# Performance work log

Measured on AMD Instinct MI355X. Metric: run time of the kernel, lower is better.

Reference implementation:

```python
import jax, jax.numpy as jnp
import numpy as np

# ---- Cl(4,1) blade algebra (CGA for 3D Euclidean space) ----
_METRIC = [1.0, 1.0, 1.0, 1.0, -1.0]  # e1..e4 square +1, e5 squares -1

def _popcount(x):
    return bin(x).count('1')

def _blade_mul(a, b):
    # sign from reordering basis vectors into canonical order
    s = 0
    t = a >> 1
    while t:
        s += _popcount(t & b)
        t >>= 1
    sign = -1.0 if (s & 1) else 1.0
    shared = a & b
    for i in range(5):
        if (shared >> i) & 1:
            sign *= _METRIC[i]
    return a ^ b, sign

_EVEN = [b for b in range(32) if _popcount(b) % 2 == 0]   # 16 even blades (versor)
_ODD = [b for b in range(32) if _popcount(b) % 2 == 1]    # 16 odd blades
_G1 = [1, 2, 4, 8, 16]                                    # grade-1 blades (CGA point)
_ODD_IDX = {b: i for i, b in enumerate(_ODD)}
_G1_IDX = {b: i for i, b in enumerate(_G1)}

def _rev_sign(b):
    g = _popcount(b)
    return -1.0 if (g * (g - 1) // 2) % 2 else 1.0

# Sparse Cayley structure tensors for the sandwich product M X ~M
_T1 = np.zeros((16, 5, 16), np.float32)   # even * grade1 -> odd
for _ie, _a in enumerate(_EVEN):
    for _ip, _b in enumerate(_G1):
        _c, _s = _blade_mul(_a, _b)
        _T1[_ie, _ip, _ODD_IDX[_c]] = _s
_T2 = np.zeros((16, 16, 5), np.float32)   # odd * reverse(even) -> grade-1
for _io, _a in enumerate(_ODD):
    for _ie, _b in enumerate(_EVEN):
        _c, _s = _blade_mul(_a, _b)
        if _c in _G1_IDX:
            _T2[_io, _ie, _G1_IDX[_c]] = _s * _rev_sign(_b)
T1 = jnp.asarray(_T1)
T2 = jnp.asarray(_T2)

N_POINTS = 2097152  # 2^21 points

def setup_inputs() -> dict:
    key = jax.random.key(0)
    k1, k2 = jax.random.split(key)
    x = jax.random.normal(k1, (N_POINTS, 3), dtype=jnp.float32)
    versor = 0.1 * jax.random.normal(k2, (N_POINTS, 16), dtype=jnp.float32)
    versor = versor.at[:, 0].add(1.0)  # near-identity even versor (scalar blade is index 0)
    return {"versor": versor, "x": x}

def _cga_encode(x):
    # P = x + 0.5|x|^2 e_inf + e_0, with e_inf = e4+e5, e_0 = (e5-e4)/2
    half_sq = 0.5 * jnp.sum(x * x, axis=-1, keepdims=True)
    return jnp.concatenate([x, half_sq - 0.5, half_sq + 0.5], axis=-1)  # (..., 5)

def _sandwich(versor, point):
    mx = jnp.einsum('...e,...p,epo->...o', versor, point, T1)   # M X : odd, 16 comps
    return jnp.einsum('...o,...e,oeq->...q', mx, versor, T2)    # (M X) ~M : grade-1, 5 comps

def _cga_decode(p):
    # scale = -P . e_inf = p[e5] - p[e4]; euclidean = P_xyz / scale
    s = p[..., 4:5] - p[..., 3:4]
    return p[..., :3] / s

def reference(versor, x):
    original_dtype = x.dtype
    xf = x.astype(jnp.float32)
    vf = versor.astype(jnp.float32)
    point = _cga_encode(xf)
    transformed = _sandwich(vf, point)
    return _cga_decode(transformed).astype(original_dtype)
```

## Files before the change

kernel.cpp:

```cpp
#include <hip/hip_runtime.h>
#include <utility>


namespace cga {

__host__ __device__ constexpr int popc5(int x) {
    int c = 0;
    for (int i = 0; i < 5; ++i) c += (x >> i) & 1;
    return c;
}
__host__ __device__ constexpr int blade_of_even(int idx) {
    int cnt = 0;
    for (int b = 0; b < 32; ++b)
        if ((popc5(b) & 1) == 0) { if (cnt == idx) return b; ++cnt; }
    return 0;
}
__host__ __device__ constexpr int blade_of_odd(int idx) {
    int cnt = 0;
    for (int b = 0; b < 32; ++b)
        if ((popc5(b) & 1) == 1) { if (cnt == idx) return b; ++cnt; }
    return 0;
}
__host__ __device__ constexpr int even_index(int blade) {
    int idx = 0;
    for (int b = 0; b < blade; ++b) if ((popc5(b) & 1) == 0) ++idx;
    return idx;
}
__host__ __device__ constexpr int odd_index(int blade) {
    int idx = 0;
    for (int b = 0; b < blade; ++b) if ((popc5(b) & 1) == 1) ++idx;
    return idx;
}
__host__ __device__ constexpr int mul_sign(int a, int b) {
    int s = 0;
    for (int t = a >> 1; t; t >>= 1) s += popc5(t & b);
    int sign = (s & 1) ? -1 : 1;
    if ((a & b) & 16) sign = -sign;
    return sign;
}
__host__ __device__ constexpr int rev_sign(int b) {
    int g = popc5(b);
    return ((g * (g - 1) / 2) & 1) ? -1 : 1;
}

struct Tables {
    int t1_dst[16][5];
    int t1_sgn[16][5];
    int t2_e[16][5];
    int t2_sgn[16][5];
};

__host__ __device__ constexpr Tables make_tables() {
    Tables r{};
    for (int ie = 0; ie < 16; ++ie) {
        const int a = blade_of_even(ie);
        for (int ip = 0; ip < 5; ++ip) {
            const int b = 1 << ip;
            const int c = a ^ b;
            r.t1_dst[ie][ip] = odd_index(c);
            r.t1_sgn[ie][ip] = mul_sign(a, b);
        }
    }
    for (int io = 0; io < 16; ++io) {
        const int a = blade_of_odd(io);
        for (int iq = 0; iq < 5; ++iq) {
            const int c = 1 << iq;
            const int b = a ^ c;
            r.t2_e[io][iq]   = even_index(b);
            r.t2_sgn[io][iq] = mul_sign(a, b) * rev_sign(b);
        }
    }
    return r;
}

constexpr Tables TAB = make_tables();

}

template <int IE, int IP>
__device__ __forceinline__ void t1_term(const float (&v)[16], const float (&p)[5],
                                        float (&mx)[16]) {
    constexpr int dst = cga::TAB.t1_dst[IE][IP];
    constexpr int sgn = cga::TAB.t1_sgn[IE][IP];
    if constexpr (sgn >= 0) mx[dst] = __builtin_fmaf( v[IE], p[IP], mx[dst]);
    else                    mx[dst] = __builtin_fmaf(-v[IE], p[IP], mx[dst]);
}
template <std::size_t... I>
__device__ __forceinline__ void t1_all(const float (&v)[16], const float (&p)[5],
                                       float (&mx)[16], std::index_sequence<I...>) {
    (t1_term<(int)(I / 5), (int)(I % 5)>(v, p, mx), ...);
}
template <int IO, int IQ>
__device__ __forceinline__ void t2_term(const float (&v)[16], const float (&mx)[16],
                                        float (&q)[5]) {
    constexpr int e   = cga::TAB.t2_e[IO][IQ];
    constexpr int sgn = cga::TAB.t2_sgn[IO][IQ];
    if constexpr (sgn >= 0) q[IQ] = __builtin_fmaf( mx[IO], v[e], q[IQ]);
    else                    q[IQ] = __builtin_fmaf(-mx[IO], v[e], q[IQ]);
}
template <std::size_t... I>
__device__ __forceinline__ void t2_all(const float (&v)[16], const float (&mx)[16],
                                       float (&q)[5], std::index_sequence<I...>) {
    (t2_term<(int)(I / 5), (int)(I % 5)>(v, mx, q), ...);
}

__device__ __forceinline__ void cga_compute(const float (&v)[16],
                                            float x0, float x1, float x2,
                                            float& o0, float& o1, float& o2) {
    const float hs = 0.5f * (x0 * x0 + x1 * x1 + x2 * x2);
    const float p[5] = {x0, x1, x2, hs - 0.5f, hs + 0.5f};
    float mx[16] = {};
    t1_all(v, p, mx, std::make_index_sequence<16 * 5>{});
    float q[5] = {};
    t2_all(v, mx, q, std::make_index_sequence<16 * 5>{});
    const float inv = 1.0f / (q[4] - q[3]);
    o0 = q[0] * inv;
    o1 = q[1] * inv;
    o2 = q[2] * inv;
}

template <int PPT>
__global__ __launch_bounds__(256) void cga_aos_kernel(
    const float* __restrict__ versor,
    const float* __restrict__ x,
    float* __restrict__ out,
    int stride_pts)
{
    const int tid = blockIdx.x * blockDim.x + threadIdx.x;

    float4 f[PPT][4];
    float  xv[PPT][3];
#pragma unroll
    for (int k = 0; k < PPT; ++k) {
        const size_t p = (size_t)tid + (size_t)k * stride_pts;
        const float4* vp = reinterpret_cast<const float4*>(versor) + p * 4;
        f[k][0] = vp[0];
        f[k][1] = vp[1];
        f[k][2] = vp[2];
        f[k][3] = vp[3];
        xv[k][0] = x[3 * p + 0];
        xv[k][1] = x[3 * p + 1];
        xv[k][2] = x[3 * p + 2];
    }

#pragma unroll
    for (int k = 0; k < PPT; ++k) {
        const float v[16] = {f[k][0].x, f[k][0].y, f[k][0].z, f[k][0].w,
                             f[k][1].x, f[k][1].y, f[k][1].z, f[k][1].w,
                             f[k][2].x, f[k][2].y, f[k][2].z, f[k][2].w,
                             f[k][3].x, f[k][3].y, f[k][3].z, f[k][3].w};
        float o0, o1, o2;
        cga_compute(v, xv[k][0], xv[k][1], xv[k][2], o0, o1, o2);
        const size_t p = (size_t)tid + (size_t)k * stride_pts;
        out[3 * p + 0] = o0;
        out[3 * p + 1] = o1;
        out[3 * p + 2] = o2;
    }
}

__global__ __launch_bounds__(256) void cga_simple_kernel(
    const float* __restrict__ versor,
    const float* __restrict__ x,
    float* __restrict__ out,
    int n)
{
    const int i = blockIdx.x * blockDim.x + threadIdx.x;
    if (i >= n) return;
    const float4* v4 = reinterpret_cast<const float4*>(versor) + (size_t)i * 4;
    const float4 a0 = v4[0], a1 = v4[1], a2 = v4[2], a3 = v4[3];
    const float v[16] = {a0.x, a0.y, a0.z, a0.w, a1.x, a1.y, a1.z, a1.w,
                         a2.x, a2.y, a2.z, a2.w, a3.x, a3.y, a3.z, a3.w};
    float o0, o1, o2;
    cga_compute(v, x[(size_t)3 * i], x[(size_t)3 * i + 1], x[(size_t)3 * i + 2],
                o0, o1, o2);
    out[(size_t)3 * i + 0] = o0;
    out[(size_t)3 * i + 1] = o1;
    out[(size_t)3 * i + 2] = o2;
}

extern "C" void kernel_launch(void* const* d_in, const int* in_sizes, int n_in,
                              void* d_out, int out_size, void* d_ws, size_t ws_size,
                              hipStream_t stream) {
    const float* versor = (const float*)d_in[0];
    const float* x      = (const float*)d_in[1];
    float* out          = (float*)d_out;
    const int n = in_sizes[0] / 16;

    constexpr int PPT = 4;
    if (n % (256 * PPT) == 0) {
        const int threads_total = n / PPT;
        const int grid = threads_total / 256;
        cga_aos_kernel<PPT><<<grid, 256, 0, stream>>>(versor, x, out, threads_total);
    } else {
        cga_simple_kernel<<<(n + 255) / 256, 256, 0, stream>>>(versor, x, out, n);
    }
}
```

Before: 212.0 us.

## Process two adjacent points per thread with vectorized nontemporal loads and stores

Replaces the strided four-points-per-thread kernel with one where each thread handles two consecutive points. The x and output arrays are read and written as 8-byte float2 vectors instead of scalar 4-byte accesses, and all loads and stores use nontemporal hints. The aim is fewer, wider memory instructions and less cache pollution for this streaming workload. In exchange each thread does less work and there is less memory-level parallelism per thread.

New measurement: 230.1 us. 1.09x slower.

```diff
diff --git a/kernel.cpp b/kernel.cpp
--- a/kernel.cpp
+++ b/kernel.cpp
@@ -119,43 +119,49 @@
     o2 = q[2] * inv;
 }
 
-template <int PPT>
-__global__ __launch_bounds__(256) void cga_aos_kernel(
+using f32x4 = __attribute__((ext_vector_type(4))) float;
+using f32x2 = __attribute__((ext_vector_type(2))) float;
+
+__global__ __launch_bounds__(256) void cga_pair_kernel(
     const float* __restrict__ versor,
     const float* __restrict__ x,
-    float* __restrict__ out,
-    int stride_pts)
+    float* __restrict__ out)
 {
-    const int tid = blockIdx.x * blockDim.x + threadIdx.x;
-
-    float4 f[PPT][4];
-    float  xv[PPT][3];
+    const size_t g = (size_t)blockIdx.x * 256 + threadIdx.x;
+
+    const f32x4* vg = reinterpret_cast<const f32x4*>(versor);
+    const f32x2* xg = reinterpret_cast<const f32x2*>(x);
+    f32x2* og = reinterpret_cast<f32x2*>(out);
+
+    f32x4 f[8];
 #pragma unroll
-    for (int k = 0; k < PPT; ++k) {
-        const size_t p = (size_t)tid + (size_t)k * stride_pts;
-        const float4* vp = reinterpret_cast<const float4*>(versor) + p * 4;
-        f[k][0] = vp[0];
-        f[k][1] = vp[1];
-        f[k][2] = vp[2];
-        f[k][3] = vp[3];
-        xv[k][0] = x[3 * p + 0];
-        xv[k][1] = x[3 * p + 1];
-        xv[k][2] = x[3 * p + 2];
-    }
-
+    for (int j = 0; j < 8; ++j)
+        f[j] = __builtin_nontemporal_load(vg + g * 8 + j);
+    f32x2 xp[3];
 #pragma unroll
-    for (int k = 0; k < PPT; ++k) {
-        const float v[16] = {f[k][0].x, f[k][0].y, f[k][0].z, f[k][0].w,
-                             f[k][1].x, f[k][1].y, f[k][1].z, f[k][1].w,
-                             f[k][2].x, f[k][2].y, f[k][2].z, f[k][2].w,
-                             f[k][3].x, f[k][3].y, f[k][3].z, f[k][3].w};
-        float o0, o1, o2;
-        cga_compute(v, xv[k][0], xv[k][1], xv[k][2], o0, o1, o2);
-        const size_t p = (size_t)tid + (size_t)k * stride_pts;
-        out[3 * p + 0] = o0;
-        out[3 * p + 1] = o1;
-        out[3 * p + 2] = o2;
-    }
+    for (int m = 0; m < 3; ++m)
+        xp[m] = __builtin_nontemporal_load(xg + g * 3 + m);
+
+    const float v0[16] = {f[0].x, f[0].y, f[0].z, f[0].w,
+                          f[1].x, f[1].y, f[1].z, f[1].w,
+                          f[2].x, f[2].y, f[2].z, f[2].w,
+                          f[3].x, f[3].y, f[3].z, f[3].w};
+    float a0, a1, a2;
+    cga_compute(v0, xp[0].x, xp[0].y, xp[1].x, a0, a1, a2);
+
+    const float v1[16] = {f[4].x, f[4].y, f[4].z, f[4].w,
+                          f[5].x, f[5].y, f[5].z, f[5].w,
+                          f[6].x, f[6].y, f[6].z, f[6].w,
+                          f[7].x, f[7].y, f[7].z, f[7].w};
+    float b0, b1, b2;
+    cga_compute(v1, xp[1].y, xp[2].x, xp[2].y, b0, b1, b2);
+
+    f32x2 s0; s0.x = a0; s0.y = a1;
+    f32x2 s1; s1.x = a2; s1.y = b0;
+    f32x2 s2; s2.x = b1; s2.y = b2;
+    __builtin_nontemporal_store(s0, og + g * 3 + 0);
+    __builtin_nontemporal_store(s1, og + g * 3 + 1);
+    __builtin_nontemporal_store(s2, og + g * 3 + 2);
 }
 
 __global__ __launch_bounds__(256) void cga_simple_kernel(
@@ -186,11 +192,9 @@
     float* out          = (float*)d_out;
     const int n = in_sizes[0] / 16;
 
-    constexpr int PPT = 4;
-    if (n % (256 * PPT) == 0) {
-        const int threads_total = n / PPT;
-        const int grid = threads_total / 256;
-        cga_aos_kernel<PPT><<<grid, 256, 0, stream>>>(versor, x, out, threads_total);
+    if ((n & 511) == 0) {
+        const int pairs = n / 2;
+        cga_pair_kernel<<<pairs / 256, 256, 0, stream>>>(versor, x, out);
     } else {
         cga_simple_kernel<<<(n + 255) / 256, 256, 0, stream>>>(versor, x, out, n);
     }
```
